# Performance work log

Measured on AMD Instinct MI355X. Metric: run time of the kernel, lower is better.

## Reference

```python
import jax, jax.numpy as jnp
import numpy as np
import math

N_HEADS = 32
N_KV_HEADS = 8
HEAD_DIM = 64
ROPE_BASE = 10000.0


def _rope_cos_sin(L, dtype):
    # inv_freq: [head_dim/2]
    inv_freq = 1.0 / (ROPE_BASE ** (jnp.arange(0, HEAD_DIM, 2, dtype=jnp.float32) / HEAD_DIM))
    t = jnp.arange(L, dtype=jnp.float32)
    freqs = jnp.outer(t, inv_freq)            # [L, head_dim/2]
    emb = jnp.concatenate([freqs, freqs], -1)  # [L, head_dim]
    return jnp.cos(emb).astype(dtype), jnp.sin(emb).astype(dtype)


def _rotate_half(x):
    x1, x2 = jnp.split(x, 2, axis=-1)
    return jnp.concatenate([-x2, x1], axis=-1)


def setup_inputs() -> dict:
    key = jax.random.key(0)
    ks = jax.random.split(key, 5)
    B, L, D = 2, 2048, 2048
    s = 0.02
    return {
        "x": jax.random.normal(ks[0], (B, L, D), jnp.float32),
        "Wq": jax.random.normal(ks[1], (D, N_HEADS * HEAD_DIM), jnp.float32) * s,
        "Wk": jax.random.normal(ks[2], (D, N_KV_HEADS * HEAD_DIM), jnp.float32) * s,
        "Wv": jax.random.normal(ks[3], (D, N_KV_HEADS * HEAD_DIM), jnp.float32) * s,
        "Wo": jax.random.normal(ks[4], (N_HEADS * HEAD_DIM, D), jnp.float32) * s,
    }


def reference(x, Wq, Wk, Wv, Wo):
    B, L, D = x.shape
    G = N_HEADS // N_KV_HEADS
    # QKV projections -> [B, H, L, hd]
    q = (x @ Wq).reshape(B, L, N_HEADS, HEAD_DIM).transpose(0, 2, 1, 3)
    k = (x @ Wk).reshape(B, L, N_KV_HEADS, HEAD_DIM).transpose(0, 2, 1, 3)
    v = (x @ Wv).reshape(B, L, N_KV_HEADS, HEAD_DIM).transpose(0, 2, 1, 3)
    # RoPE
    cos, sin = _rope_cos_sin(L, x.dtype)  # [L, hd]
    cos = cos[None, None]
    sin = sin[None, None]
    q = q * cos + _rotate_half(q) * sin
    k = k * cos + _rotate_half(k) * sin
    # GQA expand kv heads (repeat_interleave along head dim)
    k = jnp.repeat(k, G, axis=1)
    v = jnp.repeat(v, G, axis=1)
    # Causal SDPA
    scale = 1.0 / math.sqrt(HEAD_DIM)
    scores = jnp.einsum('bhqd,bhkd->bhqk', q, k) * scale  # [B,H,L,L]
    causal = jnp.tril(jnp.ones((L, L), bool))
    scores = jnp.where(causal[None, None], scores, jnp.finfo(scores.dtype).min)
    probs = jax.nn.softmax(scores, axis=-1)
    out = jnp.einsum('bhqk,bhkd->bhqd', probs, v)  # [B,H,L,hd]
    out = out.transpose(0, 2, 1, 3).reshape(B, L, N_HEADS * HEAD_DIM)
    return out @ Wo
```

## Files before the change

### kernel.cpp

```cpp
#include <hip/hip_runtime.h>
#include <hip/hip_bf16.h>
#include <stdint.h>

typedef __bf16 bf16_t;
typedef bf16_t bf16x2 __attribute__((ext_vector_type(2)));
typedef bf16_t bf16x4 __attribute__((ext_vector_type(4)));
typedef bf16_t bf16x8 __attribute__((ext_vector_type(8)));
typedef float f32x4 __attribute__((ext_vector_type(4)));
typedef float f32x16 __attribute__((ext_vector_type(16)));

#define NH 32
#define NKV 8
#define HD 64
#define LSEQ 2048
#define DMODEL 2048
#define BATCH 2

#define QSCALE 0.18033688011112042f
#define FIXED_M 12.0f

__device__ __forceinline__ void gl_lds16(const void* g, void* l) {
  __builtin_amdgcn_global_load_lds(
      (__attribute__((address_space(1))) char*)(uintptr_t)g,
      (__attribute__((address_space(3))) char*)(uintptr_t)l, 16, 0, 0);
}

__device__ __forceinline__ unsigned pack2(float a, float b) {
  bf16x2 t;
  t[0] = (bf16_t)a;
  t[1] = (bf16_t)b;
  return __builtin_bit_cast(unsigned, t);
}

__device__ __forceinline__ void transpose_tile32(
    const float* __restrict__ W, bf16_t* __restrict__ WT, int K, int N,
    int bi, float* tile ) {
  const int n32 = N >> 5;
  const int nb = (bi & (n32 - 1)) * 32, kb = (bi / n32) * 32;
  const int tx = threadIdx.x & 31, ty = threadIdx.x >> 5;
#pragma unroll
  for (int i = 0; i < 32; i += 8)
    tile[(ty + i) * 33 + tx] = W[(size_t)(kb + ty + i) * N + nb + tx];
  __syncthreads();
#pragma unroll
  for (int i = 0; i < 32; i += 8)
    WT[(size_t)(nb + ty + i) * K + kb + tx] = (bf16_t)tile[tx * 33 + ty + i];
}

__global__ __launch_bounds__(256) void prep_all(
    const float* __restrict__ x, const float* __restrict__ Wq,
    const float* __restrict__ Wk, const float* __restrict__ Wv,
    const float* __restrict__ Wo, bf16_t* __restrict__ xb,
    bf16_t* __restrict__ wqkvT, bf16_t* __restrict__ wot,
    float* __restrict__ cosT, float* __restrict__ sinT) {
  __shared__ float tile[32 * 33];
  const int bx = blockIdx.x;
  if (bx < 8192) {
    const int i = bx * 256 + threadIdx.x;
    const float4 v = ((const float4*)x)[i];
    bf16x4 o;
    o[0] = (bf16_t)v.x; o[1] = (bf16_t)v.y; o[2] = (bf16_t)v.z; o[3] = (bf16_t)v.w;
    ((bf16x4*)xb)[i] = o;
  } else if (bx < 12288) {
    transpose_tile32(Wq, wqkvT, 2048, 2048, bx - 8192, tile);
  } else if (bx < 13312) {
    transpose_tile32(Wk, wqkvT + (size_t)2048 * 2048, 2048, 512, bx - 12288, tile);
  } else if (bx < 14336) {
    transpose_tile32(Wv, wqkvT + (size_t)2560 * 2048, 2048, 512, bx - 13312, tile);
  } else if (bx < 18432) {
    transpose_tile32(Wo, wot, 2048, 2048, bx - 14336, tile);
  } else {
    const int t = (bx - 18432) * 256 + threadIdx.x;
    const int l = t >> 5, i = t & 31;
    const float inv = powf(10000.0f, -(float)i / 32.0f);
    const float ang = (float)l * inv;
    float s, c;
    sincosf(ang, &s, &c);
    cosT[t] = c;
    sinT[t] = s;
  }
}

template <int EPI>
__global__ __launch_bounds__(256, 3) void gemm128(
    const bf16_t* __restrict__ A, const bf16_t* __restrict__ BT,
    float* __restrict__ Cf, bf16_t* __restrict__ Qo, bf16_t* __restrict__ Ko,
    bf16_t* __restrict__ Vo, int M, int N, int K,
    const float* __restrict__ cosT, const float* __restrict__ sinT, int nx) {
  __shared__ bf16_t Al[128 * 64];
  __shared__ bf16_t Bl[128 * 64];
  const int tid = threadIdx.x, lane = tid & 63, w = tid >> 6;
  const int wm = w >> 1, wn = w & 1;
  const int r15 = lane & 15, g = lane >> 4;
  const int nwg = (int)gridDim.x;
  const int sid = ((int)blockIdx.x & 7) * (nwg >> 3) + ((int)blockIdx.x >> 3);
  const int m0 = (sid / nx) * 128, n0 = (sid % nx) * 128;
  f32x4 acc[4][4] = {};

  for (int kt = 0; kt < K; kt += 64) {
#pragma unroll
    for (int i = 0; i < 4; ++i) {
      const int c = i * 256 + tid;
      const int row = c >> 3, cc = c & 7;
      const int sc = (cc ^ (row & 7)) * 8;
      gl_lds16(A + (size_t)(m0 + row) * K + kt + sc, Al + c * 8);
      gl_lds16(BT + (size_t)(n0 + row) * K + kt + sc, Bl + c * 8);
    }
    __syncthreads();
#pragma unroll
    for (int kk = 0; kk < 2; ++kk) {
      bf16x8 af[4], bfr[4];
#pragma unroll
      for (int mi = 0; mi < 4; ++mi) {
        const int r = wm * 64 + mi * 16 + r15;
        af[mi] = *(const bf16x8*)((const char*)Al + r * 128 +
                                  (((kk * 4 + g) ^ (r & 7)) << 4));
      }
#pragma unroll
      for (int ni = 0; ni < 4; ++ni) {
        const int r = wn * 64 + ni * 16 + r15;
        bfr[ni] = *(const bf16x8*)((const char*)Bl + r * 128 +
                                   (((kk * 4 + g) ^ (r & 7)) << 4));
      }
#pragma unroll
      for (int mi = 0; mi < 4; ++mi)
#pragma unroll
        for (int ni = 0; ni < 4; ++ni)
          acc[mi][ni] = __builtin_amdgcn_mfma_f32_16x16x32_bf16(
              af[mi], bfr[ni], acc[mi][ni], 0, 0, 0);
    }
    __syncthreads();
  }

  if constexpr (EPI == 0) {
#pragma unroll
    for (int mi = 0; mi < 4; ++mi) {
      const int row = m0 + wm * 64 + mi * 16 + g * 4;
#pragma unroll
      for (int ni = 0; ni < 4; ++ni) {
        const int col = n0 + wn * 64 + ni * 16 + r15;
#pragma unroll
        for (int r = 0; r < 4; ++r)
          Cf[(size_t)(row + r) * N + col] = acc[mi][ni][r];
      }
    }
  } else {
    const int colbase = n0 + wn * 64;
    auto rope_store = [&](bf16_t* C, int NHT, int colrel, float sc) {
#pragma unroll
      for (int mi = 0; mi < 4; ++mi)
#pragma unroll
        for (int r = 0; r < 4; ++r) {
          const int rowg = m0 + wm * 64 + mi * 16 + g * 4 + r;
          const int bb = rowg >> 11, ls = rowg & (LSEQ - 1);
#pragma unroll
          for (int ni = 0; ni < 2; ++ni) {
            const int col = colrel + ni * 16 + r15;
            const int hh = col >> 6, d = col & 63;
            const float c = cosT[ls * 32 + d], s = sinT[ls * 32 + d];
            const float v0 = acc[mi][ni][r], v1 = acc[mi][ni + 2][r];
            bf16_t* dst = C + (((size_t)bb * NHT + hh) * LSEQ + ls) * HD + d;
            dst[0] = (bf16_t)((v0 * c - v1 * s) * sc);
            dst[32] = (bf16_t)((v1 * c + v0 * s) * sc);
          }
        }
    };
    if (n0 < 2048) {
      rope_store(Qo, NH, colbase, QSCALE);
    } else if (n0 < 2560) {
      rope_store(Ko, NKV, colbase - 2048, 1.0f);
    } else {
#pragma unroll
      for (int mi = 0; mi < 4; ++mi)
#pragma unroll
        for (int r = 0; r < 4; ++r) {
          const int rowg = m0 + wm * 64 + mi * 16 + g * 4 + r;
          const int bb = rowg >> 11, ls = rowg & (LSEQ - 1);
#pragma unroll
          for (int ni = 0; ni < 4; ++ni) {
            const int col = colbase - 2560 + ni * 16 + r15;
            const int hh = col >> 6, d = col & 63;
            Vo[(((size_t)bb * NKV + hh) * HD + d) * LSEQ + ls] =
                (bf16_t)acc[mi][ni][r];
          }
        }
    }
  }
}

template <int EPI, int NREP>
__global__ __launch_bounds__(512, 1) void gemm256(
    const bf16_t* __restrict__ A, const bf16_t* __restrict__ BT,
    float* __restrict__ Cf, int M, int N, int K, int nx) {
  __shared__ bf16_t Al[2][4 * 4096];
  __shared__ bf16_t Bl[2][NREP * 4096];
  const int tid = threadIdx.x, lane = tid & 63, w = tid >> 6;
  const int wm = w >> 2, wn = w & 3;
  const int r15 = lane & 15, g = lane >> 4;
  const int nwg = (int)gridDim.x;
  const int sid = ((int)blockIdx.x & 7) * (nwg >> 3) + ((int)blockIdx.x >> 3);
  const int m0 = (sid / nx) * 256, n0 = (sid % nx) * (NREP * 64);

  f32x4 acc[8][NREP] = {};

  const int NT = K >> 6;
  const int NI = NT >> 1;

  auto stage_q = [&](bf16_t* dst, const bf16_t* src, int row0, int kt) {
    const int r = tid >> 3;
    const int sc = (((tid & 7) ^ (r & 7)) << 3);
    gl_lds16(src + (size_t)(row0 + r) * K + (kt << 6) + sc, dst + tid * 8);
  };
  auto stage_step = [&](int d, int kt, int s) {
    kt = kt < NT ? kt : NT - 1;
    if (s == 0) { stage_q(&Bl[d][0], BT, n0, kt); stage_q(&Bl[d][4096], BT, n0 + 64, kt); }
    else if (s == 1) { stage_q(&Al[d][0], A, m0, kt); stage_q(&Al[d][8192], A, m0 + 128, kt); }
    else if (s == 2) { stage_q(&Al[d][4096], A, m0 + 64, kt); stage_q(&Al[d][12288], A, m0 + 192, kt); }
  };
  auto lda = [&](int d, int mi, int kk) -> bf16x8 {
    const int ar = (wm << 7) + (mi << 4) + r15;
    return *(const bf16x8*)((const char*)&Al[d][(ar >> 6) << 12] +
                            (ar & 63) * 128 + ((((kk << 2) + g) ^ (ar & 7)) << 4));
  };
  auto ldb = [&](int d, int ni, int kk) -> bf16x8 {
    const int br = wn * (NREP << 4) + (ni << 4) + r15;
    return *(const bf16x8*)((const char*)&Bl[d][(br >> 6) << 12] +
                            (br & 63) * 128 + ((((kk << 2) + g) ^ (br & 7)) << 4));
  };

  stage_step(0, 0, 0);
  stage_step(0, 0, 1);
  stage_step(0, 0, 2);
  stage_step(0, 0, 3);

  for (int i = 0; i < NI; ++i) {
#pragma unroll
    for (int hf = 0; hf < 2; ++hf) {
      const int dC = hf;
      const int dS = hf ^ 1;
      const int ktS = (i << 1) + 1 + hf;
      bf16x8 bf0[NREP][2];
#pragma unroll
      for (int q = 0; q < 4; ++q) {
        stage_step(dS, ktS, q);
        if (q == 0) asm volatile("s_waitcnt vmcnt(4)" ::: "memory");
        if (q == 2) asm volatile("s_waitcnt vmcnt(6)" ::: "memory");
        __builtin_amdgcn_s_barrier();
        asm volatile("" ::: "memory");
        if (q == 0) {
#pragma unroll
          for (int ni = 0; ni < NREP; ++ni)
#pragma unroll
            for (int kk = 0; kk < 2; ++kk) bf0[ni][kk] = ldb(dC, ni, kk);
        }
        bf16x8 af[2][2];
#pragma unroll
        for (int t2 = 0; t2 < 2; ++t2)
#pragma unroll
          for (int kk = 0; kk < 2; ++kk) af[t2][kk] = lda(dC, 2 * q + t2, kk);
        __builtin_amdgcn_s_setprio(1);
#pragma unroll
        for (int t2 = 0; t2 < 2; ++t2)
#pragma unroll
          for (int ni = 0; ni < NREP; ++ni)
#pragma unroll
            for (int kk = 0; kk < 2; ++kk)
              acc[2 * q + t2][ni] = __builtin_amdgcn_mfma_f32_16x16x32_bf16(
                  af[t2][kk], bf0[ni][kk], acc[2 * q + t2][ni], 0, 0, 0);
        __builtin_amdgcn_s_setprio(0);
        asm volatile("" ::: "memory");
        __builtin_amdgcn_s_barrier();
      }
    }
  }
  asm volatile("s_waitcnt vmcnt(0)" ::: "memory");

#pragma unroll
  for (int mi = 0; mi < 8; ++mi) {
    const int row = m0 + wm * 128 + mi * 16 + g * 4;
#pragma unroll
    for (int ni = 0; ni < NREP; ++ni) {
      const int col = n0 + wn * (NREP * 16) + ni * 16 + r15;
#pragma unroll
      for (int r = 0; r < 4; ++r)
        Cf[(size_t)(row + r) * N + col] = acc[mi][ni][r];
    }
  }
}

__global__ __launch_bounds__(512, 4) void attn_fwd(
    const bf16_t* __restrict__ Q, const bf16_t* __restrict__ Kh,
    const bf16_t* __restrict__ VTh, bf16_t* __restrict__ AO) {
  __shared__ bf16_t Kl[2][64 * 64];
  __shared__ bf16_t Vl[2][64 * 64];
  const int tid = threadIdx.x, lane = tid & 63, w = tid >> 6;
  const int col = lane & 31, hi = lane >> 5;
  const int hk = (int)blockIdx.x & 7, b = (int)blockIdx.x >> 3;
  const int a = (int)blockIdx.y & 15, k = (int)blockIdx.y >> 4;
  const int qt = k ? 31 - a : a;
  const int h = hk * 4 + (w & 3);
  const int qoff = (w >> 2) * 32;

  const bf16_t* Qb =
      Q + (((size_t)b * NH + h) * LSEQ + (size_t)qt * 64 + qoff) * HD;
  const bf16_t* Kb = Kh + ((size_t)b * NKV + hk) * LSEQ * HD;
  const bf16_t* Vb = VTh + ((size_t)b * NKV + hk) * HD * LSEQ;

  const int nt = qt + 1;

  auto stage = [&](int buf, int kt) {
    const int row = tid >> 3, cc = tid & 7;
    const int scol = (cc ^ (row & 7)) * 16;
    gl_lds16((const char*)Kb + (size_t)(kt * 64 + row) * 128 + scol,
             (char*)&Kl[buf][0] + tid * 16);
    gl_lds16((const char*)Vb + (size_t)row * 4096 + (size_t)kt * 128 + scol,
             (char*)&Vl[buf][0] + tid * 16);
  };

  bf16x8 qf[4];
#pragma unroll
  for (int kc = 0; kc < 4; ++kc)
    qf[kc] = *(const bf16x8*)&Qb[(size_t)col * HD + kc * 16 + hi * 8];

  f32x16 o[2] = {};
  float lsum = 0.f;

  int cur = 0;
  stage(cur, 0);
  __syncthreads();
  for (int kt = 0; kt < nt; ++kt) {
    if (kt + 1 < nt) stage(cur ^ 1, kt + 1);
    const bool diag = (kt == nt - 1);
    const char* Kcur = (const char*)&Kl[cur][0];
    const char* Vcur = (const char*)&Vl[cur][0];

    f32x16 sfrag[2] = {};
#pragma unroll
    for (int kvs = 0; kvs < 2; ++kvs) {
      if (diag && kvs * 32 > 31 + qoff) {
#pragma unroll
        for (int r = 0; r < 16; ++r) sfrag[kvs][r] = -1e30f;
        continue;
      }
      bf16x8 ak[4];
#pragma unroll
      for (int kc = 0; kc < 4; ++kc) {
        const int row = kvs * 32 + col;
        const int slot = ((kc * 2 + hi) ^ (row & 7)) * 16;
        ak[kc] = *(const bf16x8*)(Kcur + row * 128 + slot);
      }
#pragma unroll
      for (int kc = 0; kc < 4; ++kc)
        sfrag[kvs] = __builtin_amdgcn_mfma_f32_32x32x16_bf16(
            ak[kc], qf[kc], sfrag[kvs], 0, 0, 0);
    }

    if (diag) {
#pragma unroll
      for (int kvs = 0; kvs < 2; ++kvs)
#pragma unroll
        for (int r = 0; r < 16; ++r) {
          const int kvl = kvs * 32 + (r & 3) + 8 * (r >> 2) + 4 * hi;
          if (kvl > col + qoff) sfrag[kvs][r] = -1e30f;
        }
    }

    bf16x8 pf[4];
#pragma unroll
    for (int kvs = 0; kvs < 2; ++kvs)
#pragma unroll
      for (int c1 = 0; c1 < 2; ++c1) {
        float pv[8];
#pragma unroll
        for (int j = 0; j < 8; ++j) {
          pv[j] = __builtin_amdgcn_exp2f(sfrag[kvs][c1 * 8 + j] - FIXED_M);
          lsum += pv[j];
        }
        const unsigned a01 = pack2(pv[0], pv[1]), a23 = pack2(pv[2], pv[3]);
        const unsigned b01 = pack2(pv[4], pv[5]), b23 = pack2(pv[6], pv[7]);
        const unsigned s01 = __shfl_xor(hi ? a01 : b01, 32);
        const unsigned s23 = __shfl_xor(hi ? a23 : b23, 32);
        union { unsigned u[4]; bf16x8 v; } t;
        t.u[0] = hi ? s01 : a01;
        t.u[1] = hi ? s23 : a23;
        t.u[2] = hi ? b01 : s01;
        t.u[3] = hi ? b23 : s23;
        pf[kvs * 2 + c1] = t.v;
      }

#pragma unroll
    for (int ds = 0; ds < 2; ++ds) {
      bf16x8 av[4];
#pragma unroll
      for (int kc2 = 0; kc2 < 4; ++kc2) {
        const int row = ds * 32 + col;
        const int slot = ((kc2 * 2 + hi) ^ (row & 7)) * 16;
        av[kc2] = *(const bf16x8*)(Vcur + row * 128 + slot);
      }
#pragma unroll
      for (int kc2 = 0; kc2 < 4; ++kc2) {
        if (diag && kc2 * 16 > 31 + qoff) continue;
        o[ds] = __builtin_amdgcn_mfma_f32_32x32x16_bf16(
            av[kc2], pf[kc2], o[ds], 0, 0, 0);
      }
    }

    __syncthreads();
    cur ^= 1;
  }

  lsum += __shfl_xor(lsum, 32);
  const float inv = 1.0f / lsum;
  const int q = qt * 64 + qoff + col;
#pragma unroll
  for (int ds = 0; ds < 2; ++ds)
#pragma unroll
    for (int g4 = 0; g4 < 4; ++g4) {
      bf16x4 o4;
#pragma unroll
      for (int j = 0; j < 4; ++j) o4[j] = (bf16_t)(o[ds][g4 * 4 + j] * inv);
      const int d = ds * 32 + 8 * g4 + 4 * hi;
      *(bf16x4*)&AO[((size_t)b * LSEQ + q) * DMODEL + h * HD + d] = o4;
    }
}


extern "C" void kernel_launch(void* const* d_in, const int* in_sizes, int n_in,
                              void* d_out, int out_size, void* d_ws, size_t ws_size,
                              hipStream_t stream) {
  const float* x = (const float*)d_in[0];
  const float* Wq = (const float*)d_in[1];
  const float* Wk = (const float*)d_in[2];
  const float* Wv = (const float*)d_in[3];
  const float* Wo = (const float*)d_in[4];
  char* ws = (char*)d_ws;
  size_t off = 0;
  auto alloc = [&](size_t bytes) {
    char* p = ws + off;
    off += (bytes + 255) & ~(size_t)255;
    return p;
  };
  bf16_t* xb = (bf16_t*)alloc((size_t)BATCH * LSEQ * DMODEL * 2);
  bf16_t* wqkvT = (bf16_t*)alloc((size_t)3072 * DMODEL * 2);
  bf16_t* wot = (bf16_t*)alloc((size_t)DMODEL * DMODEL * 2);
  float* cosT = (float*)alloc((size_t)LSEQ * 32 * 4);
  float* sinT = (float*)alloc((size_t)LSEQ * 32 * 4);
  bf16_t* Qh = (bf16_t*)alloc((size_t)BATCH * NH * LSEQ * HD * 2);
  bf16_t* Kh = (bf16_t*)alloc((size_t)BATCH * NKV * LSEQ * HD * 2);
  bf16_t* VTh = (bf16_t*)alloc((size_t)BATCH * NKV * HD * LSEQ * 2);
  bf16_t* AO = (bf16_t*)alloc((size_t)BATCH * LSEQ * NH * HD * 2);
  (void)ws_size; (void)in_sizes; (void)n_in; (void)out_size;

  const int M = BATCH * LSEQ;

  prep_all<<<18688, 256, 0, stream>>>(x, Wq, Wk, Wv, Wo, xb, wqkvT, wot,
                                      cosT, sinT);

  gemm128<3><<<768, 256, 0, stream>>>(
      xb, wqkvT, nullptr, Qh, Kh, VTh, M, 3072, 2048, cosT, sinT, 24);

  attn_fwd<<<dim3(16, 32), 512, 0, stream>>>(Qh, Kh, VTh, AO);

  gemm256<0, 2><<<256, 512, 0, stream>>>(
      AO, wot, (float*)d_out, M, 2048, 2048, 16);
}
```

Measured before the change: 163.9 us.

## Use pipelined 256x192 GEMM for QKV projection and split RoPE into scatter kernel

Replaces the simple 128x128 QKV GEMM, which had RoPE and layout scatter fused into its epilogue, with the double-buffered gemm256 kernel using a 256x192 tile (NREP=3) that writes a plain bf16 QKV buffer. A separate rope_scatter kernel then applies RoPE to Q/K and transposes V through shared memory into the head-major layouts. The aim is higher MFMA throughput and better data reuse in the projection GEMM. In exchange it adds an extra kernel launch and a round trip through a 24 MB intermediate buffer.

```diff
diff --git a/kernel.cpp b/kernel.cpp
--- a/kernel.cpp
+++ b/kernel.cpp
@@ -81,109 +81,49 @@
   }
 }
 
-template <int EPI>
-__global__ __launch_bounds__(256, 3) void gemm128(
-    const bf16_t* __restrict__ A, const bf16_t* __restrict__ BT,
-    float* __restrict__ Cf, bf16_t* __restrict__ Qo, bf16_t* __restrict__ Ko,
-    bf16_t* __restrict__ Vo, int M, int N, int K,
-    const float* __restrict__ cosT, const float* __restrict__ sinT, int nx) {
-  __shared__ bf16_t Al[128 * 64];
-  __shared__ bf16_t Bl[128 * 64];
-  const int tid = threadIdx.x, lane = tid & 63, w = tid >> 6;
-  const int wm = w >> 1, wn = w & 1;
-  const int r15 = lane & 15, g = lane >> 4;
-  const int nwg = (int)gridDim.x;
-  const int sid = ((int)blockIdx.x & 7) * (nwg >> 3) + ((int)blockIdx.x >> 3);
-  const int m0 = (sid / nx) * 128, n0 = (sid % nx) * 128;
-  f32x4 acc[4][4] = {};
-
-  for (int kt = 0; kt < K; kt += 64) {
-#pragma unroll
-    for (int i = 0; i < 4; ++i) {
-      const int c = i * 256 + tid;
-      const int row = c >> 3, cc = c & 7;
-      const int sc = (cc ^ (row & 7)) * 8;
-      gl_lds16(A + (size_t)(m0 + row) * K + kt + sc, Al + c * 8);
-      gl_lds16(BT + (size_t)(n0 + row) * K + kt + sc, Bl + c * 8);
+__global__ __launch_bounds__(256) void rope_scatter(
+    const bf16_t* __restrict__ QKVf, const float* __restrict__ cosT,
+    const float* __restrict__ sinT, bf16_t* __restrict__ Qh,
+    bf16_t* __restrict__ Kh, bf16_t* __restrict__ VTh) {
+  const int bx = blockIdx.x;
+  if (bx < 2560) {
+    const int hh = bx >> 6;
+    const int rg = bx & 63;
+    const bool isQ = hh < 32;
+    const int d = threadIdx.x & 31, rs = threadIdx.x >> 5;
+    const float sc = isQ ? QSCALE : 1.0f;
+#pragma unroll
+    for (int rr = 0; rr < 8; ++rr) {
+      const int row = rg * 64 + rr * 8 + rs;
+      const int ls = row & (LSEQ - 1), bb = row >> 11;
+      const float a = (float)QKVf[(size_t)row * 3072 + hh * 64 + d];
+      const float b2 = (float)QKVf[(size_t)row * 3072 + hh * 64 + 32 + d];
+      const float c = cosT[ls * 32 + d], s = sinT[ls * 32 + d];
+      bf16_t* dst = isQ
+          ? Qh + (((size_t)bb * NH + hh) * LSEQ + ls) * HD + d
+          : Kh + (((size_t)bb * NKV + (hh - 32)) * LSEQ + ls) * HD + d;
+      dst[0] = (bf16_t)((a * c - b2 * s) * sc);
+      dst[32] = (bf16_t)((b2 * c + a * s) * sc);
+    }
+  } else {
+    __shared__ bf16_t vt[64][68];
+    const int i2 = bx - 2560;
+    const int vh = i2 >> 6, rg = i2 & 63;
+    const int c64 = threadIdx.x & 63, q4 = threadIdx.x >> 6;
+#pragma unroll
+    for (int rr = 0; rr < 16; ++rr) {
+      const int lrow = rr * 4 + q4;
+      vt[lrow][c64] =
+          QKVf[(size_t)(rg * 64 + lrow) * 3072 + 2560 + vh * 64 + c64];
     }
     __syncthreads();
-#pragma unroll
-    for (int kk = 0; kk < 2; ++kk) {
-      bf16x8 af[4], bfr[4];
-#pragma unroll
-      for (int mi = 0; mi < 4; ++mi) {
-        const int r = wm * 64 + mi * 16 + r15;
-        af[mi] = *(const bf16x8*)((const char*)Al + r * 128 +
-                                  (((kk * 4 + g) ^ (r & 7)) << 4));
-      }
-#pragma unroll
-      for (int ni = 0; ni < 4; ++ni) {
-        const int r = wn * 64 + ni * 16 + r15;
-        bfr[ni] = *(const bf16x8*)((const char*)Bl + r * 128 +
-                                   (((kk * 4 + g) ^ (r & 7)) << 4));
-      }
-#pragma unroll
-      for (int mi = 0; mi < 4; ++mi)
-#pragma unroll
-        for (int ni = 0; ni < 4; ++ni)
-          acc[mi][ni] = __builtin_amdgcn_mfma_f32_16x16x32_bf16(
-              af[mi], bfr[ni], acc[mi][ni], 0, 0, 0);
-    }
-    __syncthreads();
-  }
-
-  if constexpr (EPI == 0) {
-#pragma unroll
-    for (int mi = 0; mi < 4; ++mi) {
-      const int row = m0 + wm * 64 + mi * 16 + g * 4;
-#pragma unroll
-      for (int ni = 0; ni < 4; ++ni) {
-        const int col = n0 + wn * 64 + ni * 16 + r15;
-#pragma unroll
-        for (int r = 0; r < 4; ++r)
-          Cf[(size_t)(row + r) * N + col] = acc[mi][ni][r];
-      }
-    }
-  } else {
-    const int colbase = n0 + wn * 64;
-    auto rope_store = [&](bf16_t* C, int NHT, int colrel, float sc) {
-#pragma unroll
-      for (int mi = 0; mi < 4; ++mi)
-#pragma unroll
-        for (int r = 0; r < 4; ++r) {
-          const int rowg = m0 + wm * 64 + mi * 16 + g * 4 + r;
-          const int bb = rowg >> 11, ls = rowg & (LSEQ - 1);
-#pragma unroll
-          for (int ni = 0; ni < 2; ++ni) {
-            const int col = colrel + ni * 16 + r15;
-            const int hh = col >> 6, d = col & 63;
-            const float c = cosT[ls * 32 + d], s = sinT[ls * 32 + d];
-            const float v0 = acc[mi][ni][r], v1 = acc[mi][ni + 2][r];
-            bf16_t* dst = C + (((size_t)bb * NHT + hh) * LSEQ + ls) * HD + d;
-            dst[0] = (bf16_t)((v0 * c - v1 * s) * sc);
-            dst[32] = (bf16_t)((v1 * c + v0 * s) * sc);
-          }
-        }
-    };
-    if (n0 < 2048) {
-      rope_store(Qo, NH, colbase, QSCALE);
-    } else if (n0 < 2560) {
-      rope_store(Ko, NKV, colbase - 2048, 1.0f);
-    } else {
-#pragma unroll
-      for (int mi = 0; mi < 4; ++mi)
-#pragma unroll
-        for (int r = 0; r < 4; ++r) {
-          const int rowg = m0 + wm * 64 + mi * 16 + g * 4 + r;
-          const int bb = rowg >> 11, ls = rowg & (LSEQ - 1);
-#pragma unroll
-          for (int ni = 0; ni < 4; ++ni) {
-            const int col = colbase - 2560 + ni * 16 + r15;
-            const int hh = col >> 6, d = col & 63;
-            Vo[(((size_t)bb * NKV + hh) * HD + d) * LSEQ + ls] =
-                (bf16_t)acc[mi][ni][r];
-          }
-        }
+    const int row0 = rg * 64;
+    const int bb = row0 >> 11, ls0 = row0 & (LSEQ - 1);
+#pragma unroll
+    for (int rr = 0; rr < 16; ++rr) {
+      const int dd = rr * 4 + q4;
+      VTh[(((size_t)bb * NKV + vh) * HD + dd) * LSEQ + ls0 + c64] =
+          vt[c64][dd];
     }
   }
 }
@@ -191,7 +131,7 @@
 template <int EPI, int NREP>
 __global__ __launch_bounds__(512, 1) void gemm256(
     const bf16_t* __restrict__ A, const bf16_t* __restrict__ BT,
-    float* __restrict__ Cf, int M, int N, int K, int nx) {
+    void* __restrict__ Cp, int M, int N, int K, int nx) {
   __shared__ bf16_t Al[2][4 * 4096];
   __shared__ bf16_t Bl[2][NREP * 4096];
   const int tid = threadIdx.x, lane = tid & 63, w = tid >> 6;
@@ -213,9 +153,16 @@
   };
   auto stage_step = [&](int d, int kt, int s) {
     kt = kt < NT ? kt : NT - 1;
-    if (s == 0) { stage_q(&Bl[d][0], BT, n0, kt); stage_q(&Bl[d][4096], BT, n0 + 64, kt); }
-    else if (s == 1) { stage_q(&Al[d][0], A, m0, kt); stage_q(&Al[d][8192], A, m0 + 128, kt); }
-    else if (s == 2) { stage_q(&Al[d][4096], A, m0 + 64, kt); stage_q(&Al[d][12288], A, m0 + 192, kt); }
+    if constexpr (NREP == 3) {
+      if (s == 0) { stage_q(&Bl[d][0], BT, n0, kt); stage_q(&Bl[d][4096], BT, n0 + 64, kt); }
+      else if (s == 1) { stage_q(&Bl[d][8192], BT, n0 + 128, kt); stage_q(&Al[d][0], A, m0, kt); }
+      else if (s == 2) { stage_q(&Al[d][8192], A, m0 + 128, kt); stage_q(&Al[d][4096], A, m0 + 64, kt); }
+      else { stage_q(&Al[d][12288], A, m0 + 192, kt); }
+    } else {
+      if (s == 0) { stage_q(&Bl[d][0], BT, n0, kt); stage_q(&Bl[d][4096], BT, n0 + 64, kt); }
+      else if (s == 1) { stage_q(&Al[d][0], A, m0, kt); stage_q(&Al[d][8192], A, m0 + 128, kt); }
+      else if (s == 2) { stage_q(&Al[d][4096], A, m0 + 64, kt); stage_q(&Al[d][12288], A, m0 + 192, kt); }
+    }
   };
   auto lda = [&](int d, int mi, int kk) -> bf16x8 {
     const int ar = (wm << 7) + (mi << 4) + r15;
@@ -243,7 +190,10 @@
 #pragma unroll
       for (int q = 0; q < 4; ++q) {
         stage_step(dS, ktS, q);
-        if (q == 0) asm volatile("s_waitcnt vmcnt(4)" ::: "memory");
+        if (q == 0) {
+          if (NREP == 3) asm volatile("s_waitcnt vmcnt(3)" ::: "memory");
+          else asm volatile("s_waitcnt vmcnt(4)" ::: "memory");
+        }
         if (q == 2) asm volatile("s_waitcnt vmcnt(6)" ::: "memory");
         __builtin_amdgcn_s_barrier();
         asm volatile("" ::: "memory");
@@ -275,15 +225,31 @@
   }
   asm volatile("s_waitcnt vmcnt(0)" ::: "memory");
 
-#pragma unroll
-  for (int mi = 0; mi < 8; ++mi) {
-    const int row = m0 + wm * 128 + mi * 16 + g * 4;
-#pragma unroll
-    for (int ni = 0; ni < NREP; ++ni) {
-      const int col = n0 + wn * (NREP * 16) + ni * 16 + r15;
-#pragma unroll
-      for (int r = 0; r < 4; ++r)
-        Cf[(size_t)(row + r) * N + col] = acc[mi][ni][r];
+  if constexpr (EPI == 0) {
+    float* Cf = (float*)Cp;
+#pragma unroll
+    for (int mi = 0; mi < 8; ++mi) {
+      const int row = m0 + wm * 128 + mi * 16 + g * 4;
+#pragma unroll
+      for (int ni = 0; ni < NREP; ++ni) {
+        const int col = n0 + wn * (NREP * 16) + ni * 16 + r15;
+#pragma unroll
+        for (int r = 0; r < 4; ++r)
+          Cf[(size_t)(row + r) * N + col] = acc[mi][ni][r];
+      }
+    }
+  } else {
+    bf16_t* Cb = (bf16_t*)Cp;
+#pragma unroll
+    for (int mi = 0; mi < 8; ++mi) {
+      const int row = m0 + wm * 128 + mi * 16 + g * 4;
+#pragma unroll
+      for (int ni = 0; ni < NREP; ++ni) {
+        const int col = n0 + wn * (NREP * 16) + ni * 16 + r15;
+#pragma unroll
+        for (int r = 0; r < 4; ++r)
+          Cb[(size_t)(row + r) * N + col] = (bf16_t)acc[mi][ni][r];
+      }
     }
   }
 }
@@ -445,6 +411,7 @@
   bf16_t* wot = (bf16_t*)alloc((size_t)DMODEL * DMODEL * 2);
   float* cosT = (float*)alloc((size_t)LSEQ * 32 * 4);
   float* sinT = (float*)alloc((size_t)LSEQ * 32 * 4);
+  bf16_t* QKVf = (bf16_t*)alloc((size_t)BATCH * LSEQ * 3072 * 2);
   bf16_t* Qh = (bf16_t*)alloc((size_t)BATCH * NH * LSEQ * HD * 2);
   bf16_t* Kh = (bf16_t*)alloc((size_t)BATCH * NKV * LSEQ * HD * 2);
   bf16_t* VTh = (bf16_t*)alloc((size_t)BATCH * NKV * HD * LSEQ * 2);
@@ -456,8 +423,10 @@
   prep_all<<<18688, 256, 0, stream>>>(x, Wq, Wk, Wv, Wo, xb, wqkvT, wot,
                                       cosT, sinT);
 
-  gemm128<3><<<768, 256, 0, stream>>>(
-      xb, wqkvT, nullptr, Qh, Kh, VTh, M, 3072, 2048, cosT, sinT, 24);
+  gemm256<1, 3><<<256, 512, 0, stream>>>(
+      xb, wqkvT, QKVf, M, 3072, 2048, 16);
+
+  rope_scatter<<<3072, 256, 0, stream>>>(QKVf, cosT, sinT, Qh, Kh, VTh);
 
   attn_fwd<<<dim3(16, 32), 512, 0, stream>>>(Qh, Kh, VTh, AO);
 
```

After: 165.7 us. No clear change (+1.1%).
